# Kernel optimization log

Hardware: AMD Instinct MI355X
Metric: run time of the kernel (lower is better)

## Reference

```python
import jax, jax.numpy as jnp
import numpy as np

NU, NS, NM = 80000, 20000, 30000
D = 128
E_UI, E_MM = 1_500_000, 480_000
B, L = 2048, 32
LAYERS = 2


def spmm(rows, cols, vals, x, n):
    # sparse [n,n] @ dense [n,d] via gather + segment_sum
    return jax.ops.segment_sum(vals[:, None] * x[cols], rows, num_segments=n)


def setup_inputs() -> dict:
    key = jax.random.key(0)
    ks = jax.random.split(key, 20)
    inp = {}
    inp['mashup_inputs'] = jax.random.randint(ks[0], (B,), 0, NM, dtype=jnp.int32)
    inp['service_inputs'] = jax.random.randint(ks[1], (B,), 0, NS, dtype=jnp.int32)
    inp['member_masked'] = jax.random.randint(ks[2], (B, L), 0, NU, dtype=jnp.int32)
    # variable-length compose lists: length in [1, L]; mask==1 marks padding
    lens = jax.random.randint(ks[3], (B, 1), 1, L + 1)
    inp['mask'] = (jnp.arange(L)[None, :] >= lens).astype(jnp.float32)
    inp['member_masked'] = jnp.where(inp['mask'] > 0, 0, inp['member_masked'])
    inp['adj_rows'] = jax.random.randint(ks[4], (E_UI,), 0, NU + NS, dtype=jnp.int32)
    inp['adj_cols'] = jax.random.randint(ks[5], (E_UI,), 0, NU + NS, dtype=jnp.int32)
    inp['adj_vals'] = jax.random.uniform(ks[6], (E_UI,)) * 0.1
    inp['A_rows'] = jax.random.randint(ks[7], (E_MM,), 0, NM, dtype=jnp.int32)
    inp['A_cols'] = jax.random.randint(ks[8], (E_MM,), 0, NM, dtype=jnp.int32)
    inp['A_vals'] = jax.random.uniform(ks[9], (E_MM,)) * 0.1
    inp['d_inv'] = jax.random.uniform(ks[10], (NM,)) * 0.1
    s = 0.05
    inp['user_tbl'] = jax.random.normal(ks[11], (NU, D)) * s
    inp['service_tbl'] = jax.random.normal(ks[12], (NS, D)) * s
    inp['mashup_tbl'] = jax.random.normal(ks[13], (NM, D)) * s
    inp['att_w1'] = jax.random.normal(ks[14], (2 * D, 16)) * s
    inp['att_b1'] = jnp.zeros((16,))
    inp['att_w2'] = jax.random.normal(ks[15], (16, 1)) * s
    inp['att_b2'] = jnp.zeros((1,))
    inp['pred_w1'] = jax.random.normal(ks[16], (3 * D, 8)) * s
    inp['pred_b1'] = jnp.zeros((8,))
    inp['pred_w2'] = jax.random.normal(ks[17], (8, 1)) * s
    inp['pred_b2'] = jnp.zeros((1,))
    return inp


def reference(mashup_inputs, service_inputs, member_masked, adj_rows, adj_cols,
              A_rows, A_cols, mask, user_tbl, service_tbl, mashup_tbl,
              adj_vals, A_vals, d_inv, att_w1, att_b1, att_w2, att_b2,
              pred_w1, pred_b1, pred_w2, pred_b2):
    # HyperConv on concatenated user+service embeddings (layer-mean aggregation)
    ui = jnp.concatenate([user_tbl, service_tbl], axis=0)  # [NU+NS, D]
    acc, h = ui, ui
    for _ in range(LAYERS):
        h = spmm(adj_rows, adj_cols, adj_vals, h, NU + NS)
        acc = acc + h
    ui = acc / (LAYERS + 1)
    user_e, service_e = ui[:NU], ui[NU:]
    service_emb = service_e[service_inputs]  # [B, D]

    # HyperConv2 on mashup graph: emb <- D^-1 A emb per layer, layer-mean
    acc, m = mashup_tbl, mashup_tbl
    for _ in range(LAYERS):
        m = d_inv[:, None] * spmm(A_rows, A_cols, A_vals, m, NM)
        acc = acc + m
    mashup_embedding = acc / (LAYERS + 1)

    # ragged gather + masked attention pooling over compose members
    member_emb = user_e[member_masked]                      # [B, L, D]
    svc_exp = jnp.broadcast_to(service_emb[:, None, :], (B, L, D))
    at_emb = jnp.concatenate([member_emb, svc_exp], axis=2)  # [B, L, 2D]
    hdn = jax.nn.relu(at_emb @ att_w1 + att_b1)             # [B, L, 16]
    scores = (hdn @ att_w2 + att_b2)[..., 0]                 # [B, L]
    scores = jnp.where(mask > 0, -1e9, scores)               # mask padding
    at_wt = jax.nn.softmax(scores, axis=1)
    g_att = jnp.einsum('bl,bld->bd', at_wt, member_emb)      # [B, D]

    mashup_emb = g_att + mashup_embedding[mashup_inputs]
    elem = mashup_emb * service_emb
    new_emb = jnp.concatenate([elem, mashup_emb, service_emb], axis=1)  # [B, 3D]
    hp = jax.nn.relu(new_emb @ pred_w1 + pred_b1)
    y = jax.nn.sigmoid(hp @ pred_w2 + pred_b2)               # [B, 1]
    return y
```

## Files before the change

### kernel.cpp

```cpp
#include <hip/hip_runtime.h>
#include <climits>

#define NU_ 80000
#define NS_ 20000
#define NM_ 30000
#define UIN_ (NU_ + NS_)
#define DD 128
#define LL 32
#define RPB 64
#define NCH 256
#define NBUK_UI ((UIN_ + RPB - 1) / RPB)
#define NBUK_MM ((NM_  + RPB - 1) / RPB)

#define F8_SCALE 512.0f
#define F8_INV   (1.0f / 512.0f)

typedef unsigned int   uint32;
typedef unsigned short ushort_t;
typedef unsigned char  uchar_t;
typedef float f32x2 __attribute__((ext_vector_type(2)));

__device__ __forceinline__ float bflo(uint32 u) { return __uint_as_float(u << 16); }
__device__ __forceinline__ float bfhi(uint32 u) { return __uint_as_float(u & 0xffff0000u); }
__device__ __forceinline__ uint32 f2bf(float f) {
    uint32 u = __float_as_uint(f);
    return (u + 0x7fffu + ((u >> 16) & 1u)) >> 16;
}
__device__ __forceinline__ uint32 pack2bf(float lo, float hi) {
    return f2bf(lo) | (f2bf(hi) << 16);
}

__device__ __forceinline__ float dec1_f8(uint32 b) {
    uint32 em = b & 0x7fu;
    uint32 s  = (b & 0x80u) << 24;
    float vn = __uint_as_float(s | (((em >> 3) + 120u) << 23) | ((em & 7u) << 20));
    float vd = (float)(int)em * 0.001953125f;
    vd = (b & 0x80u) ? -vd : vd;
    return (em >= 8u) ? vn : vd;
}
__device__ __forceinline__ uint32 enc1_f8(float f) {
    uint32 u = __float_as_uint(f);
    uint32 s = (u >> 31) << 7;
    float a = fabsf(f);
    if (a >= 448.0f) return s | 0x7Eu;
    if (a < 0.015625f) {
        int m = (int)(a * 512.0f + 0.5f);
        return s | (uint32)m;
    }
    uint32 au = u & 0x7fffffffu;
    au += 0x7FFFFu + ((au >> 20) & 1u);
    uint32 em = (((au >> 23) - 120u) << 3) | ((au >> 20) & 7u);
    if (em >= 0x7Fu) em = 0x7Eu;
    return s | em;
}
__device__ __forceinline__ f32x2 dec2_f8(uint32 u) {
#if __has_builtin(__builtin_amdgcn_cvt_pk_f32_fp8)
    return __builtin_amdgcn_cvt_pk_f32_fp8(u, false);
#else
    f32x2 r; r.x = dec1_f8(u & 0xffu); r.y = dec1_f8((u >> 8) & 0xffu); return r;
#endif
}
__device__ __forceinline__ f32x2 dec2_f8_hi(uint32 u) {
#if __has_builtin(__builtin_amdgcn_cvt_pk_f32_fp8)
    return __builtin_amdgcn_cvt_pk_f32_fp8(u, true);
#else
    f32x2 r; r.x = dec1_f8((u >> 16) & 0xffu); r.y = dec1_f8(u >> 24); return r;
#endif
}
__device__ __forceinline__ uint32 pack2f8(float lo, float hi) {
#if __has_builtin(__builtin_amdgcn_cvt_pk_fp8_f32)
    return (uint32)__builtin_amdgcn_cvt_pk_fp8_f32(lo, hi, 0, false) & 0xFFFFu;
#else
    return enc1_f8(lo) | (enc1_f8(hi) << 8);
#endif
}

__global__ void convert_fused(const float* __restrict__ user_tbl,
                              const float* __restrict__ service_tbl,
                              const float* __restrict__ mashup_tbl,
                              uint32* __restrict__ ui_bf, ushort_t* __restrict__ ui_f8,
                              uint32* __restrict__ mash_bf, ushort_t* __restrict__ mash_f8) {
    const size_t P_UI = (size_t)UIN_ * 64;
    const size_t P_MM = (size_t)NM_ * 64;
    const size_t SPLIT = (size_t)NU_ * DD;
    size_t stride = (size_t)gridDim.x * blockDim.x;
    for (size_t i = (size_t)blockIdx.x * blockDim.x + threadIdx.x; i < P_UI + P_MM; i += stride) {
        if (i < P_UI) {
            size_t e = i * 2;
            const float* s = (e < SPLIT) ? (user_tbl + e) : (service_tbl + (e - SPLIT));
            float2 v = *reinterpret_cast<const float2*>(s);
            ui_bf[i] = pack2bf(v.x, v.y);
            ui_f8[i] = (ushort_t)pack2f8(v.x * F8_SCALE, v.y * F8_SCALE);
        } else {
            size_t j = i - P_UI;
            float2 v = *reinterpret_cast<const float2*>(mashup_tbl + j * 2);
            mash_bf[j] = pack2bf(v.x, v.y);
            mash_f8[j] = (ushort_t)pack2f8(v.x * F8_SCALE, v.y * F8_SCALE);
        }
    }
}

__global__ __launch_bounds__(1024) void hist_fused(
    const int* __restrict__ rows_ui, int E_ui, int csz_ui, int* __restrict__ h_ui,
    const int* __restrict__ rows_mm, int E_mm, int csz_mm, int* __restrict__ h_mm) {
    __shared__ int hist[NBUK_UI];
    const int* rows; int E, csz, nbuk, c; int* h;
    if ((int)blockIdx.x < NCH) { rows = rows_ui; E = E_ui; csz = csz_ui; h = h_ui; nbuk = NBUK_UI; c = blockIdx.x; }
    else                       { rows = rows_mm; E = E_mm; csz = csz_mm; h = h_mm; nbuk = NBUK_MM; c = blockIdx.x - NCH; }
    for (int i = threadIdx.x; i < nbuk; i += 1024) hist[i] = 0;
    __syncthreads();
    const int lo = c * csz, hi = min(lo + csz, E);
    int i = lo + threadIdx.x;
    for (; i + 3 * 1024 < hi; i += 4 * 1024) {
        int r0 = rows[i];
        int r1 = rows[i + 1024];
        int r2 = rows[i + 2048];
        int r3 = rows[i + 3072];
        atomicAdd(&hist[r0 >> 6], 1);
        atomicAdd(&hist[r1 >> 6], 1);
        atomicAdd(&hist[r2 >> 6], 1);
        atomicAdd(&hist[r3 >> 6], 1);
    }
    for (; i < hi; i += 1024) atomicAdd(&hist[rows[i] >> 6], 1);
    __syncthreads();
    for (int b = threadIdx.x; b < nbuk; b += 1024)
        h[b * NCH + c] = hist[b];
}

__global__ __launch_bounds__(256) void scan_blocksum_fused(
    const int* __restrict__ h_ui, int n_ui, int* __restrict__ bs_ui, int nb_ui,
    const int* __restrict__ h_mm, int n_mm, int* __restrict__ bs_mm) {
    __shared__ int red[256];
    const int* cnt; int n, b; int* bsum;
    if ((int)blockIdx.x < nb_ui) { cnt = h_ui; n = n_ui; bsum = bs_ui; b = blockIdx.x; }
    else                         { cnt = h_mm; n = n_mm; bsum = bs_mm; b = blockIdx.x - nb_ui; }
    int base = b * 1024 + threadIdx.x * 4;
    int s = 0;
    if (base + 3 < n) {
        int4 v = *reinterpret_cast<const int4*>(cnt + base);
        s = v.x + v.y + v.z + v.w;
    } else {
        for (int i = base; i < n && i < base + 4; ++i) s += cnt[i];
    }
    red[threadIdx.x] = s;
    __syncthreads();
    for (int off = 128; off >= 1; off >>= 1) {
        if (threadIdx.x < off) red[threadIdx.x] += red[threadIdx.x + off];
        __syncthreads();
    }
    if (threadIdx.x == 0) bsum[b] = red[0];
}

__global__ __launch_bounds__(256) void scan_final_fused(
    int* __restrict__ h_ui, int n_ui, const int* __restrict__ bs_ui, int nb_ui,
    int* __restrict__ s_ui,
    int* __restrict__ h_mm, int n_mm, const int* __restrict__ bs_mm,
    int* __restrict__ s_mm) {
    __shared__ int lds[256];
    __shared__ int blk_off_s;
    const int tid = threadIdx.x;
    int* cnt; int n, b; const int* bsum; int* row_ptr;
    if ((int)blockIdx.x < nb_ui) { cnt = h_ui; n = n_ui; bsum = bs_ui; row_ptr = s_ui; b = blockIdx.x; }
    else                         { cnt = h_mm; n = n_mm; bsum = bs_mm; row_ptr = s_mm; b = blockIdx.x - nb_ui; }

    int s = 0;
    for (int j = tid; j < b; j += 256) s += bsum[j];
    lds[tid] = s;
    __syncthreads();
    for (int off = 128; off >= 1; off >>= 1) {
        if (tid < off) lds[tid] += lds[tid + off];
        __syncthreads();
    }
    if (tid == 0) blk_off_s = lds[0];
    __syncthreads();
    const int blk_off = blk_off_s;

    int base = b * 1024 + tid * 4;
    int c0 = 0, c1 = 0, c2 = 0, c3 = 0;
    if (base + 3 < n) {
        int4 v = *reinterpret_cast<const int4*>(cnt + base);
        c0 = v.x; c1 = v.y; c2 = v.z; c3 = v.w;
    } else {
        if (base     < n) c0 = cnt[base];
        if (base + 1 < n) c1 = cnt[base + 1];
        if (base + 2 < n) c2 = cnt[base + 2];
        if (base + 3 < n) c3 = cnt[base + 3];
    }
    int tsum = c0 + c1 + c2 + c3;
    __syncthreads();
    lds[tid] = tsum;
    __syncthreads();
    for (int off = 1; off < 256; off <<= 1) {
        int v = (tid >= off) ? lds[tid - off] : 0;
        __syncthreads();
        lds[tid] += v;
        __syncthreads();
    }
    int p0 = blk_off + ((tid > 0) ? lds[tid - 1] : 0);
    int p1 = p0 + c0, p2 = p1 + c1, p3 = p2 + c2, p4 = p3 + c3;

    if (base     < n) { row_ptr[base]     = p0; if (base     == n - 1) row_ptr[n] = p1; }
    if (base + 1 < n) { row_ptr[base + 1] = p1; if (base + 1 == n - 1) row_ptr[n] = p2; }
    if (base + 2 < n) { row_ptr[base + 2] = p2; if (base + 2 == n - 1) row_ptr[n] = p3; }
    if (base + 3 < n) { row_ptr[base + 3] = p3; if (base + 3 == n - 1) row_ptr[n] = p4; }
}

__global__ __launch_bounds__(1024) void scatter_fused(
    const int* __restrict__ rows_ui, const int* __restrict__ cols_ui,
    const float* __restrict__ vals_ui, const int* __restrict__ s_ui,
    int E_ui, int csz_ui, uint2* __restrict__ cvA_ui,
    const int* __restrict__ rows_mm, const int* __restrict__ cols_mm,
    const float* __restrict__ vals_mm, const int* __restrict__ s_mm,
    int E_mm, int csz_mm, uint2* __restrict__ cvA_mm) {
    __shared__ int cur[NBUK_UI];
    const int *rows, *cols; const float* vals; const int* s;
    int E, csz, nbuk, c; uint2* cvA;
    if ((int)blockIdx.x < NCH) {
        rows = rows_ui; cols = cols_ui; vals = vals_ui; s = s_ui;
        E = E_ui; csz = csz_ui; nbuk = NBUK_UI; c = blockIdx.x; cvA = cvA_ui;
    } else {
        rows = rows_mm; cols = cols_mm; vals = vals_mm; s = s_mm;
        E = E_mm; csz = csz_mm; nbuk = NBUK_MM; c = blockIdx.x - NCH; cvA = cvA_mm;
    }
    for (int b = threadIdx.x; b < nbuk; b += 1024) cur[b] = s[b * NCH + c];
    __syncthreads();
    const int lo = c * csz, hi = min(lo + csz, E);
    int i = lo + threadIdx.x;
    for (; i + 3 * 1024 < hi; i += 4 * 1024) {
        int   r0 = rows[i],        r1 = rows[i + 1024];
        int   r2 = rows[i + 2048], r3 = rows[i + 3072];
        int   q0 = cols[i],        q1 = cols[i + 1024];
        int   q2 = cols[i + 2048], q3 = cols[i + 3072];
        float v0 = vals[i],        v1 = vals[i + 1024];
        float v2 = vals[i + 2048], v3 = vals[i + 3072];
        int p0 = atomicAdd(&cur[r0 >> 6], 1);
        int p1 = atomicAdd(&cur[r1 >> 6], 1);
        int p2 = atomicAdd(&cur[r2 >> 6], 1);
        int p3 = atomicAdd(&cur[r3 >> 6], 1);
        cvA[p0] = make_uint2((uint32)q0 | ((uint32)(r0 & 63) << 25), __float_as_uint(v0));
        cvA[p1] = make_uint2((uint32)q1 | ((uint32)(r1 & 63) << 25), __float_as_uint(v1));
        cvA[p2] = make_uint2((uint32)q2 | ((uint32)(r2 & 63) << 25), __float_as_uint(v2));
        cvA[p3] = make_uint2((uint32)q3 | ((uint32)(r3 & 63) << 25), __float_as_uint(v3));
    }
    for (; i < hi; i += 1024) {
        int r = rows[i];
        int pos = atomicAdd(&cur[r >> 6], 1);
        cvA[pos] = make_uint2((uint32)cols[i] | ((uint32)(r & 63) << 25),
                              __float_as_uint(vals[i]));
    }
}

__device__ __forceinline__ void sort_one_bucket(
    const uint2* __restrict__ cvA, const int* __restrict__ s,
    uint2* __restrict__ cvB, int* __restrict__ row_ptr, int nrows, int b,
    int* cnt, int* cur) {
    const int tid  = threadIdx.x;
    const int base = s[b * NCH];
    const int endb = s[(b + 1) * NCH];

    if (tid < RPB) cnt[tid] = 0;
    __syncthreads();
    for (int i = base + tid; i < endb; i += 256)
        atomicAdd(&cnt[cvA[i].x >> 25], 1);
    __syncthreads();
    if (tid < 64) {
        int c = cnt[tid];
        int x = c;
        #pragma unroll
        for (int off = 1; off < 64; off <<= 1) {
            int v = __shfl_up(x, off);
            if (tid >= off) x += v;
        }
        int excl = base + x - c;
        cur[tid] = excl;
        int grow = b * RPB + tid;
        if (grow <= nrows) row_ptr[grow] = excl;
    }
    __syncthreads();
    for (int i = base + tid; i < endb; i += 256) {
        uint2 e = cvA[i];
        int rl  = (int)(e.x >> 25);
        int pos = atomicAdd(&cur[rl], 1);
        cvB[pos] = make_uint2(e.x & 0x1FFFFFFu, e.y);
    }
}

__global__ __launch_bounds__(256) void sort_fused(
    const uint2* __restrict__ cvA_ui, const int* __restrict__ s_ui,
    uint2* __restrict__ cvB_ui, int* __restrict__ rp_ui,
    const uint2* __restrict__ cvA_mm, const int* __restrict__ s_mm,
    uint2* __restrict__ cvB_mm, int* __restrict__ rp_mm) {
    __shared__ int cnt[RPB];
    __shared__ int cur[RPB];
    if ((int)blockIdx.x < NBUK_UI)
        sort_one_bucket(cvA_ui, s_ui, cvB_ui, rp_ui, UIN_, blockIdx.x, cnt, cur);
    else
        sort_one_bucket(cvA_mm, s_mm, cvB_mm, rp_mm, NM_, blockIdx.x - NBUK_UI, cnt, cur);
}

template <int MODE>
__device__ __forceinline__ void pull_row(
    const int wid, const int lane,
    const int* __restrict__ row_ptr, const uint2* __restrict__ cv,
    const uchar_t* __restrict__ x, const float* __restrict__ d_inv,
    const uint32* __restrict__ orig_bf, const uchar_t* __restrict__ hprev_f8,
    void* __restrict__ out)
{
    const int q    = lane >> 4;
    const int ql   = lane & 15;
    const int beg  = row_ptr[wid];
    const int end  = row_ptr[wid + 1];
    const int boff = ql << 3;

    float a0 = 0.f, a1 = 0.f, a2 = 0.f, a3 = 0.f;
    float a4 = 0.f, a5 = 0.f, a6 = 0.f, a7 = 0.f;

    int e = beg + q;
    for (; e + 12 < end; e += 16) {
        uint2 p0 = cv[e],     p1 = cv[e + 4];
        uint2 p2 = cv[e + 8], p3 = cv[e + 12];
        uint2 g0 = *reinterpret_cast<const uint2*>(x + (((size_t)p0.x) << 7) + boff);
        uint2 g1 = *reinterpret_cast<const uint2*>(x + (((size_t)p1.x) << 7) + boff);
        uint2 g2 = *reinterpret_cast<const uint2*>(x + (((size_t)p2.x) << 7) + boff);
        uint2 g3 = *reinterpret_cast<const uint2*>(x + (((size_t)p3.x) << 7) + boff);
        float v0 = __uint_as_float(p0.y), v1 = __uint_as_float(p1.y);
        float v2 = __uint_as_float(p2.y), v3 = __uint_as_float(p3.y);
        {
            f32x2 d0 = dec2_f8(g0.x), d1 = dec2_f8_hi(g0.x);
            f32x2 d2 = dec2_f8(g0.y), d3 = dec2_f8_hi(g0.y);
            a0 += v0 * d0.x; a1 += v0 * d0.y; a2 += v0 * d1.x; a3 += v0 * d1.y;
            a4 += v0 * d2.x; a5 += v0 * d2.y; a6 += v0 * d3.x; a7 += v0 * d3.y;
        }
        {
            f32x2 d0 = dec2_f8(g1.x), d1 = dec2_f8_hi(g1.x);
            f32x2 d2 = dec2_f8(g1.y), d3 = dec2_f8_hi(g1.y);
            a0 += v1 * d0.x; a1 += v1 * d0.y; a2 += v1 * d1.x; a3 += v1 * d1.y;
            a4 += v1 * d2.x; a5 += v1 * d2.y; a6 += v1 * d3.x; a7 += v1 * d3.y;
        }
        {
            f32x2 d0 = dec2_f8(g2.x), d1 = dec2_f8_hi(g2.x);
            f32x2 d2 = dec2_f8(g2.y), d3 = dec2_f8_hi(g2.y);
            a0 += v2 * d0.x; a1 += v2 * d0.y; a2 += v2 * d1.x; a3 += v2 * d1.y;
            a4 += v2 * d2.x; a5 += v2 * d2.y; a6 += v2 * d3.x; a7 += v2 * d3.y;
        }
        {
            f32x2 d0 = dec2_f8(g3.x), d1 = dec2_f8_hi(g3.x);
            f32x2 d2 = dec2_f8(g3.y), d3 = dec2_f8_hi(g3.y);
            a0 += v3 * d0.x; a1 += v3 * d0.y; a2 += v3 * d1.x; a3 += v3 * d1.y;
            a4 += v3 * d2.x; a5 += v3 * d2.y; a6 += v3 * d3.x; a7 += v3 * d3.y;
        }
    }
    for (; e < end; e += 4) {
        uint2 pa = cv[e];
        uint2 ga = *reinterpret_cast<const uint2*>(x + (((size_t)pa.x) << 7) + boff);
        float va = __uint_as_float(pa.y);
        f32x2 d0 = dec2_f8(ga.x), d1 = dec2_f8_hi(ga.x);
        f32x2 d2 = dec2_f8(ga.y), d3 = dec2_f8_hi(ga.y);
        a0 += va * d0.x; a1 += va * d0.y; a2 += va * d1.x; a3 += va * d1.y;
        a4 += va * d2.x; a5 += va * d2.y; a6 += va * d3.x; a7 += va * d3.y;
    }

    a0 += __shfl_xor(a0, 16); a0 += __shfl_xor(a0, 32);
    a1 += __shfl_xor(a1, 16); a1 += __shfl_xor(a1, 32);
    a2 += __shfl_xor(a2, 16); a2 += __shfl_xor(a2, 32);
    a3 += __shfl_xor(a3, 16); a3 += __shfl_xor(a3, 32);
    a4 += __shfl_xor(a4, 16); a4 += __shfl_xor(a4, 32);
    a5 += __shfl_xor(a5, 16); a5 += __shfl_xor(a5, 32);
    a6 += __shfl_xor(a6, 16); a6 += __shfl_xor(a6, 32);
    a7 += __shfl_xor(a7, 16); a7 += __shfl_xor(a7, 32);

    if (lane < 16) {
        if (MODE & 1) {
            float s = d_inv[wid];
            a0 *= s; a1 *= s; a2 *= s; a3 *= s;
            a4 *= s; a5 *= s; a6 *= s; a7 *= s;
        }
        if (MODE & 2) {
            const float inv3 = 1.0f / 3.0f;
            uint4 o = *reinterpret_cast<const uint4*>(orig_bf + (size_t)wid * 64 + (ql << 2));
            uint2 hp = *reinterpret_cast<const uint2*>(hprev_f8 + (((size_t)wid) << 7) + boff);
            f32x2 h0 = dec2_f8(hp.x), h1 = dec2_f8_hi(hp.x);
            f32x2 h2 = dec2_f8(hp.y), h3 = dec2_f8_hi(hp.y);
            uint4 r;
            r.x = pack2bf((bflo(o.x) + (h0.x + a0) * F8_INV) * inv3,
                          (bfhi(o.x) + (h0.y + a1) * F8_INV) * inv3);
            r.y = pack2bf((bflo(o.y) + (h1.x + a2) * F8_INV) * inv3,
                          (bfhi(o.y) + (h1.y + a3) * F8_INV) * inv3);
            r.z = pack2bf((bflo(o.z) + (h2.x + a4) * F8_INV) * inv3,
                          (bfhi(o.z) + (h2.y + a5) * F8_INV) * inv3);
            r.w = pack2bf((bflo(o.w) + (h3.x + a6) * F8_INV) * inv3,
                          (bfhi(o.w) + (h3.y + a7) * F8_INV) * inv3);
            *reinterpret_cast<uint4*>(reinterpret_cast<uint32*>(out) + (size_t)wid * 64 + (ql << 2)) = r;
        } else {
            uint2 r;
            r.x = pack2f8(a0, a1) | (pack2f8(a2, a3) << 16);
            r.y = pack2f8(a4, a5) | (pack2f8(a6, a7) << 16);
            *reinterpret_cast<uint2*>((uchar_t*)out + (((size_t)wid) << 7) + boff) = r;
        }
    }
}

__global__ __launch_bounds__(256) void pull_L1_fused(
    const int* __restrict__ rp_ui, const uint2* __restrict__ cv_ui,
    const uchar_t* __restrict__ x_ui, uchar_t* __restrict__ out_ui,
    const int* __restrict__ rp_mm, const uint2* __restrict__ cv_mm,
    const uchar_t* __restrict__ x_mm, const float* __restrict__ d_inv,
    uchar_t* __restrict__ out_mm, int ui_blocks)
{
    const int lane = threadIdx.x & 63;
    const int w    = threadIdx.x >> 6;
    if ((int)blockIdx.x < ui_blocks) {
        int wid = blockIdx.x * 4 + w;
        if (wid < UIN_)
            pull_row<0>(wid, lane, rp_ui, cv_ui, x_ui, nullptr, nullptr, nullptr, out_ui);
    } else {
        int wid = (blockIdx.x - ui_blocks) * 4 + w;
        if (wid < NM_)
            pull_row<1>(wid, lane, rp_mm, cv_mm, x_mm, d_inv, nullptr, nullptr, out_mm);
    }
}

__global__ __launch_bounds__(256) void pull_L2_fused(
    const int* __restrict__ rp_ui, const uint2* __restrict__ cv_ui,
    const uchar_t* __restrict__ h1_f8, const uint32* __restrict__ ui_bf,
    uint32* __restrict__ h2,
    const int* __restrict__ rp_mm, const uint2* __restrict__ cv_mm,
    const uchar_t* __restrict__ m1_f8, const float* __restrict__ d_inv,
    const uint32* __restrict__ mash_bf, uint32* __restrict__ m2, int ui_blocks)
{
    const int lane = threadIdx.x & 63;
    const int w    = threadIdx.x >> 6;
    if ((int)blockIdx.x < ui_blocks) {
        int wid = blockIdx.x * 4 + w;
        if (wid < UIN_)
            pull_row<2>(wid, lane, rp_ui, cv_ui, h1_f8, nullptr, ui_bf, h1_f8, h2);
    } else {
        int wid = (blockIdx.x - ui_blocks) * 4 + w;
        if (wid < NM_)
            pull_row<3>(wid, lane, rp_mm, cv_mm, m1_f8, d_inv, mash_bf, m1_f8, m2);
    }
}

__global__ __launch_bounds__(512) void attn_pred_kernel(
    const int* __restrict__ mashup_inputs, const int* __restrict__ service_inputs,
    const int* __restrict__ member_masked, const float* __restrict__ mask,
    const uint32* __restrict__ ui_final, const uint32* __restrict__ mash_final,
    const float* __restrict__ att_w1, const float* __restrict__ att_b1,
    const float* __restrict__ att_w2, const float* __restrict__ att_b2,
    const float* __restrict__ pred_w1, const float* __restrict__ pred_b1,
    const float* __restrict__ pred_w2, const float* __restrict__ pred_b2,
    float* __restrict__ out)
{
    const int b   = blockIdx.x;
    const int tid = threadIdx.x;

    __shared__ float mem_lds[LL * 129];
    __shared__ float svc_lds[DD];
    __shared__ float mash_lds[DD];
    __shared__ float w1_lds[2 * DD * 16];
    __shared__ float hdnw_lds[LL * 16];
    __shared__ float wt_lds[LL];
    __shared__ float new_lds[3 * DD];
    __shared__ float hp_lds[8];
    __shared__ int   midx[LL];

    if (tid < LL) midx[tid] = member_masked[b * LL + tid];
    for (int i = tid; i < 2 * DD * 16; i += 512) w1_lds[i] = att_w1[i];
    if (tid < 64) {
        int sidx = service_inputs[b];
        uint32 u = ui_final[(size_t)(NU_ + sidx) * 64 + tid];
        svc_lds[tid * 2]     = bflo(u);
        svc_lds[tid * 2 + 1] = bfhi(u);
    } else if (tid >= 448) {
        int t  = tid - 448;
        int mi = mashup_inputs[b];
        uint32 u = mash_final[(size_t)mi * 64 + t];
        mash_lds[t * 2]     = bflo(u);
        mash_lds[t * 2 + 1] = bfhi(u);
    }
    __syncthreads();

    for (int i = tid; i < LL * 64; i += 512) {
        int l = i >> 6, dp = (i & 63) * 2;
        uint32 u = ui_final[(size_t)midx[l] * 64 + (i & 63)];
        mem_lds[l * 129 + dp]     = bflo(u);
        mem_lds[l * 129 + dp + 1] = bfhi(u);
    }
    __syncthreads();

    {
        int l = tid >> 4, j = tid & 15;
        float acc = att_b1[j];
        const float* m = &mem_lds[l * 129];
        #pragma unroll 4
        for (int k = 0; k < DD; ++k) acc += m[k] * w1_lds[k * 16 + j];
        #pragma unroll 4
        for (int k = 0; k < DD; ++k) acc += svc_lds[k] * w1_lds[(DD + k) * 16 + j];
        acc = fmaxf(acc, 0.0f);
        hdnw_lds[l * 16 + j] = acc * att_w2[j];
    }
    __syncthreads();

    if (tid < 64) {
        float s = -3.0e38f;
        if (tid < LL) {
            s = att_b2[0];
            for (int j = 0; j < 16; ++j) s += hdnw_lds[tid * 16 + j];
            if (mask[b * LL + tid] > 0.0f) s = -1.0e9f;
        }
        float mx = s;
        for (int off = 16; off >= 1; off >>= 1) mx = fmaxf(mx, __shfl_xor(mx, off));
        float ex = (tid < LL) ? __expf(s - mx) : 0.0f;
        float sum = ex;
        for (int off = 16; off >= 1; off >>= 1) sum += __shfl_xor(sum, off);
        if (tid < LL) wt_lds[tid] = ex / sum;
    }
    __syncthreads();

    if (tid < DD) {
        float g = 0.0f;
        #pragma unroll 4
        for (int l = 0; l < LL; ++l) g += wt_lds[l] * mem_lds[l * 129 + tid];
        float me = g + mash_lds[tid];
        float sv = svc_lds[tid];
        new_lds[tid]          = me * sv;
        new_lds[DD + tid]     = me;
        new_lds[2 * DD + tid] = sv;
    }
    __syncthreads();

    if (tid < 8) {
        float acc = pred_b1[tid];
        for (int k = 0; k < 3 * DD; ++k) acc += new_lds[k] * pred_w1[k * 8 + tid];
        acc = fmaxf(acc, 0.0f);
        hp_lds[tid] = acc * pred_w2[tid];
    }
    __syncthreads();

    if (tid == 0) {
        float z = pred_b2[0];
        for (int j = 0; j < 8; ++j) z += hp_lds[j];
        out[b] = 1.0f / (1.0f + __expf(-z));
    }
}

extern "C" void kernel_launch(void* const* d_in, const int* in_sizes, int n_in,
                              void* d_out, int out_size, void* d_ws, size_t ws_size,
                              hipStream_t stream) {
    const int*   mashup_inputs  = (const int*)  d_in[0];
    const int*   service_inputs = (const int*)  d_in[1];
    const int*   member_masked  = (const int*)  d_in[2];
    const float* mask           = (const float*)d_in[3];
    const int*   adj_rows       = (const int*)  d_in[4];
    const int*   adj_cols       = (const int*)  d_in[5];
    const float* adj_vals       = (const float*)d_in[6];
    const int*   A_rows         = (const int*)  d_in[7];
    const int*   A_cols         = (const int*)  d_in[8];
    const float* A_vals         = (const float*)d_in[9];
    const float* d_inv          = (const float*)d_in[10];
    const float* user_tbl       = (const float*)d_in[11];
    const float* service_tbl    = (const float*)d_in[12];
    const float* mashup_tbl     = (const float*)d_in[13];
    const float* att_w1         = (const float*)d_in[14];
    const float* att_b1         = (const float*)d_in[15];
    const float* att_w2         = (const float*)d_in[16];
    const float* att_b2         = (const float*)d_in[17];
    const float* pred_w1        = (const float*)d_in[18];
    const float* pred_b1        = (const float*)d_in[19];
    const float* pred_w2        = (const float*)d_in[20];
    const float* pred_b2        = (const float*)d_in[21];

    const int E_ui = in_sizes[4];
    const int E_mm = in_sizes[7];
    const int B    = in_sizes[0];

    const int N_UI2  = NBUK_UI * NCH;
    const int N_MM2  = NBUK_MM * NCH;
    const int NB_UI  = (N_UI2 + 1023) / 1024;
    const int NB_MM  = (N_MM2 + 1023) / 1024;
    const int csz_ui = (E_ui + NCH - 1) / NCH;
    const int csz_mm = (E_mm + NCH - 1) / NCH;

    uint2*   cvA_ui  = (uint2*)d_ws;
    uint2*   cvA_mm  = cvA_ui + E_ui;
    uint2*   cvB_ui  = cvA_mm + E_mm;
    uint2*   cvB_mm  = cvB_ui + E_ui;
    int*     h_ui    = (int*)(cvB_mm + E_mm);
    int*     s_ui    = h_ui + N_UI2;
    int*     h_mm    = s_ui + N_UI2 + 4;
    int*     s_mm    = h_mm + N_MM2;
    int*     bs_ui   = s_mm + N_MM2 + 4;
    int*     bs_mm   = bs_ui + 512;
    int*     rp_ui   = bs_mm + 128;
    int*     rp_mm   = rp_ui + UIN_ + 4;
    uint32*  ui_bf   = (uint32*)(rp_mm + NM_ + 4);
    uint32*  mash_bf = ui_bf + (size_t)UIN_ * 64;
    uint32*  h2      = mash_bf + (size_t)NM_ * 64;
    uint32*  m2      = h2 + (size_t)UIN_ * 64;
    uchar_t* ui_f8   = (uchar_t*)(m2 + (size_t)NM_ * 64);
    uchar_t* h1_f8   = ui_f8 + (size_t)UIN_ * DD;
    uchar_t* mash_f8 = h1_f8 + (size_t)UIN_ * DD;
    uchar_t* m1_f8   = mash_f8 + (size_t)NM_ * DD;

    convert_fused<<<2048, 256, 0, stream>>>(user_tbl, service_tbl, mashup_tbl,
                                            ui_bf, (ushort_t*)ui_f8,
                                            mash_bf, (ushort_t*)mash_f8);

    hist_fused<<<2 * NCH, 1024, 0, stream>>>(adj_rows, E_ui, csz_ui, h_ui,
                                             A_rows, E_mm, csz_mm, h_mm);
    scan_blocksum_fused<<<NB_UI + NB_MM, 256, 0, stream>>>(h_ui, N_UI2, bs_ui, NB_UI,
                                                           h_mm, N_MM2, bs_mm);
    scan_final_fused<<<NB_UI + NB_MM, 256, 0, stream>>>(h_ui, N_UI2, bs_ui, NB_UI, s_ui,
                                                        h_mm, N_MM2, bs_mm, s_mm);
    scatter_fused<<<2 * NCH, 1024, 0, stream>>>(
        adj_rows, adj_cols, adj_vals, s_ui, E_ui, csz_ui, cvA_ui,
        A_rows, A_cols, A_vals, s_mm, E_mm, csz_mm, cvA_mm);
    sort_fused<<<NBUK_UI + NBUK_MM, 256, 0, stream>>>(
        cvA_ui, s_ui, cvB_ui, rp_ui,
        cvA_mm, s_mm, cvB_mm, rp_mm);

    const int ui_blocks = (UIN_ + 3) / 4;
    const int mm_blocks = (NM_ + 3) / 4;
    pull_L1_fused<<<ui_blocks + mm_blocks, 256, 0, stream>>>(
        rp_ui, cvB_ui, ui_f8, h1_f8,
        rp_mm, cvB_mm, mash_f8, d_inv, m1_f8, ui_blocks);
    pull_L2_fused<<<ui_blocks + mm_blocks, 256, 0, stream>>>(
        rp_ui, cvB_ui, h1_f8, ui_bf, h2,
        rp_mm, cvB_mm, m1_f8, d_inv, mash_bf, m2, ui_blocks);

    attn_pred_kernel<<<B, 512, 0, stream>>>(
        mashup_inputs, service_inputs, member_masked, mask,
        h2, m2,
        att_w1, att_b1, att_w2, att_b2,
        pred_w1, pred_b1, pred_w2, pred_b2,
        (float*)d_out);
}
```

Measured before the change: 262.8 us.

## Split fused pull kernels per graph and shrink SpMM gather unroll to two

Each fused L1/L2 pull kernel, which handled both the user-item and mashup graphs in one launch, is split into separate per-graph launches (four launches instead of two). The inner gather loop in pull_row drops from 4-way to 2-way unrolling, with a single-step tail. The likely aims are lower register pressure and higher occupancy, plus simpler kernels without the block-index branch. The cost is two extra launches and less overlap between the two graphs' work, and fewer gathers in flight per wave.

```diff
diff --git a/kernel.cpp b/kernel.cpp
--- a/kernel.cpp
+++ b/kernel.cpp
@@ -316,41 +316,23 @@
     float a4 = 0.f, a5 = 0.f, a6 = 0.f, a7 = 0.f;
 
     int e = beg + q;
-    for (; e + 12 < end; e += 16) {
-        uint2 p0 = cv[e],     p1 = cv[e + 4];
-        uint2 p2 = cv[e + 8], p3 = cv[e + 12];
-        uint2 g0 = *reinterpret_cast<const uint2*>(x + (((size_t)p0.x) << 7) + boff);
-        uint2 g1 = *reinterpret_cast<const uint2*>(x + (((size_t)p1.x) << 7) + boff);
-        uint2 g2 = *reinterpret_cast<const uint2*>(x + (((size_t)p2.x) << 7) + boff);
-        uint2 g3 = *reinterpret_cast<const uint2*>(x + (((size_t)p3.x) << 7) + boff);
-        float v0 = __uint_as_float(p0.y), v1 = __uint_as_float(p1.y);
-        float v2 = __uint_as_float(p2.y), v3 = __uint_as_float(p3.y);
-        {
-            f32x2 d0 = dec2_f8(g0.x), d1 = dec2_f8_hi(g0.x);
-            f32x2 d2 = dec2_f8(g0.y), d3 = dec2_f8_hi(g0.y);
-            a0 += v0 * d0.x; a1 += v0 * d0.y; a2 += v0 * d1.x; a3 += v0 * d1.y;
-            a4 += v0 * d2.x; a5 += v0 * d2.y; a6 += v0 * d3.x; a7 += v0 * d3.y;
-        }
-        {
-            f32x2 d0 = dec2_f8(g1.x), d1 = dec2_f8_hi(g1.x);
-            f32x2 d2 = dec2_f8(g1.y), d3 = dec2_f8_hi(g1.y);
-            a0 += v1 * d0.x; a1 += v1 * d0.y; a2 += v1 * d1.x; a3 += v1 * d1.y;
-            a4 += v1 * d2.x; a5 += v1 * d2.y; a6 += v1 * d3.x; a7 += v1 * d3.y;
-        }
-        {
-            f32x2 d0 = dec2_f8(g2.x), d1 = dec2_f8_hi(g2.x);
-            f32x2 d2 = dec2_f8(g2.y), d3 = dec2_f8_hi(g2.y);
-            a0 += v2 * d0.x; a1 += v2 * d0.y; a2 += v2 * d1.x; a3 += v2 * d1.y;
-            a4 += v2 * d2.x; a5 += v2 * d2.y; a6 += v2 * d3.x; a7 += v2 * d3.y;
-        }
-        {
-            f32x2 d0 = dec2_f8(g3.x), d1 = dec2_f8_hi(g3.x);
-            f32x2 d2 = dec2_f8(g3.y), d3 = dec2_f8_hi(g3.y);
-            a0 += v3 * d0.x; a1 += v3 * d0.y; a2 += v3 * d1.x; a3 += v3 * d1.y;
-            a4 += v3 * d2.x; a5 += v3 * d2.y; a6 += v3 * d3.x; a7 += v3 * d3.y;
-        }
-    }
-    for (; e < end; e += 4) {
+    for (; e + 4 < end; e += 8) {
+        uint2 pa = cv[e];
+        uint2 pb = cv[e + 4];
+        uint2 ga = *reinterpret_cast<const uint2*>(x + (((size_t)pa.x) << 7) + boff);
+        uint2 gb = *reinterpret_cast<const uint2*>(x + (((size_t)pb.x) << 7) + boff);
+        float va = __uint_as_float(pa.y);
+        float vb = __uint_as_float(pb.y);
+        f32x2 d0 = dec2_f8(ga.x), d1 = dec2_f8_hi(ga.x);
+        f32x2 d2 = dec2_f8(ga.y), d3 = dec2_f8_hi(ga.y);
+        a0 += va * d0.x; a1 += va * d0.y; a2 += va * d1.x; a3 += va * d1.y;
+        a4 += va * d2.x; a5 += va * d2.y; a6 += va * d3.x; a7 += va * d3.y;
+        f32x2 e0 = dec2_f8(gb.x), e1 = dec2_f8_hi(gb.x);
+        f32x2 e2 = dec2_f8(gb.y), e3 = dec2_f8_hi(gb.y);
+        a0 += vb * e0.x; a1 += vb * e0.y; a2 += vb * e1.x; a3 += vb * e1.y;
+        a4 += vb * e2.x; a5 += vb * e2.y; a6 += vb * e3.x; a7 += vb * e3.y;
+    }
+    if (e < end) {
         uint2 pa = cv[e];
         uint2 ga = *reinterpret_cast<const uint2*>(x + (((size_t)pa.x) << 7) + boff);
         float va = __uint_as_float(pa.y);
@@ -400,45 +382,36 @@
     }
 }
 
-__global__ __launch_bounds__(256) void pull_L1_fused(
-    const int* __restrict__ rp_ui, const uint2* __restrict__ cv_ui,
-    const uchar_t* __restrict__ x_ui, uchar_t* __restrict__ out_ui,
-    const int* __restrict__ rp_mm, const uint2* __restrict__ cv_mm,
-    const uchar_t* __restrict__ x_mm, const float* __restrict__ d_inv,
-    uchar_t* __restrict__ out_mm, int ui_blocks)
-{
+__global__ __launch_bounds__(256) void pull_ui_l1(
+    const int* __restrict__ rp, const uint2* __restrict__ cv,
+    const uchar_t* __restrict__ x, uchar_t* __restrict__ out) {
     const int lane = threadIdx.x & 63;
-    const int w    = threadIdx.x >> 6;
-    if ((int)blockIdx.x < ui_blocks) {
-        int wid = blockIdx.x * 4 + w;
-        if (wid < UIN_)
-            pull_row<0>(wid, lane, rp_ui, cv_ui, x_ui, nullptr, nullptr, nullptr, out_ui);
-    } else {
-        int wid = (blockIdx.x - ui_blocks) * 4 + w;
-        if (wid < NM_)
-            pull_row<1>(wid, lane, rp_mm, cv_mm, x_mm, d_inv, nullptr, nullptr, out_mm);
-    }
-}
-
-__global__ __launch_bounds__(256) void pull_L2_fused(
-    const int* __restrict__ rp_ui, const uint2* __restrict__ cv_ui,
-    const uchar_t* __restrict__ h1_f8, const uint32* __restrict__ ui_bf,
-    uint32* __restrict__ h2,
-    const int* __restrict__ rp_mm, const uint2* __restrict__ cv_mm,
-    const uchar_t* __restrict__ m1_f8, const float* __restrict__ d_inv,
-    const uint32* __restrict__ mash_bf, uint32* __restrict__ m2, int ui_blocks)
-{
+    int wid = blockIdx.x * 4 + (threadIdx.x >> 6);
+    if (wid < UIN_) pull_row<0>(wid, lane, rp, cv, x, nullptr, nullptr, nullptr, out);
+}
+__global__ __launch_bounds__(256) void pull_mm_l1(
+    const int* __restrict__ rp, const uint2* __restrict__ cv,
+    const uchar_t* __restrict__ x, const float* __restrict__ d_inv,
+    uchar_t* __restrict__ out) {
     const int lane = threadIdx.x & 63;
-    const int w    = threadIdx.x >> 6;
-    if ((int)blockIdx.x < ui_blocks) {
-        int wid = blockIdx.x * 4 + w;
-        if (wid < UIN_)
-            pull_row<2>(wid, lane, rp_ui, cv_ui, h1_f8, nullptr, ui_bf, h1_f8, h2);
-    } else {
-        int wid = (blockIdx.x - ui_blocks) * 4 + w;
-        if (wid < NM_)
-            pull_row<3>(wid, lane, rp_mm, cv_mm, m1_f8, d_inv, mash_bf, m1_f8, m2);
-    }
+    int wid = blockIdx.x * 4 + (threadIdx.x >> 6);
+    if (wid < NM_) pull_row<1>(wid, lane, rp, cv, x, d_inv, nullptr, nullptr, out);
+}
+__global__ __launch_bounds__(256) void pull_ui_l2(
+    const int* __restrict__ rp, const uint2* __restrict__ cv,
+    const uchar_t* __restrict__ h1, const uint32* __restrict__ orig_bf,
+    uint32* __restrict__ out) {
+    const int lane = threadIdx.x & 63;
+    int wid = blockIdx.x * 4 + (threadIdx.x >> 6);
+    if (wid < UIN_) pull_row<2>(wid, lane, rp, cv, h1, nullptr, orig_bf, h1, out);
+}
+__global__ __launch_bounds__(256) void pull_mm_l2(
+    const int* __restrict__ rp, const uint2* __restrict__ cv,
+    const uchar_t* __restrict__ m1, const float* __restrict__ d_inv,
+    const uint32* __restrict__ orig_bf, uint32* __restrict__ out) {
+    const int lane = threadIdx.x & 63;
+    int wid = blockIdx.x * 4 + (threadIdx.x >> 6);
+    if (wid < NM_) pull_row<3>(wid, lane, rp, cv, m1, d_inv, orig_bf, m1, out);
 }
 
 __global__ __launch_bounds__(512) void attn_pred_kernel(
@@ -621,12 +594,10 @@
 
     const int ui_blocks = (UIN_ + 3) / 4;
     const int mm_blocks = (NM_ + 3) / 4;
-    pull_L1_fused<<<ui_blocks + mm_blocks, 256, 0, stream>>>(
-        rp_ui, cvB_ui, ui_f8, h1_f8,
-        rp_mm, cvB_mm, mash_f8, d_inv, m1_f8, ui_blocks);
-    pull_L2_fused<<<ui_blocks + mm_blocks, 256, 0, stream>>>(
-        rp_ui, cvB_ui, h1_f8, ui_bf, h2,
-        rp_mm, cvB_mm, m1_f8, d_inv, mash_bf, m2, ui_blocks);
+    pull_mm_l1<<<mm_blocks, 256, 0, stream>>>(rp_mm, cvB_mm, mash_f8, d_inv, m1_f8);
+    pull_ui_l1<<<ui_blocks, 256, 0, stream>>>(rp_ui, cvB_ui, ui_f8, h1_f8);
+    pull_mm_l2<<<mm_blocks, 256, 0, stream>>>(rp_mm, cvB_mm, m1_f8, d_inv, mash_bf, m2);
+    pull_ui_l2<<<ui_blocks, 256, 0, stream>>>(rp_ui, cvB_ui, h1_f8, ui_bf, h2);
 
     attn_pred_kernel<<<B, 512, 0, stream>>>(
         mashup_inputs, service_inputs, member_masked, mask,
```

After: 256.1 us. 1.03x faster.
